# Kernel optimization log

Hardware: AMD Instinct MI355X
Metric: run time of the kernel (lower is better)

Reference implementation:

```python
import jax, jax.numpy as jnp
import numpy as np

C = 256
H_HEADS = 8
HEAD_DIM = C // H_HEADS
B, H, W = 2, 64, 64


def conv1x1(x, w, b):
    # x: [B,C,H,W], w: [O,C], b: [O]
    return jnp.einsum('oc,bchw->bohw', w, x) + b[None, :, None, None]


def setup_inputs() -> dict:
    key = jax.random.key(0)
    ks = jax.random.split(key, 12)
    s = 1.0 / np.sqrt(C)
    inp = {
        'query': jax.random.normal(ks[0], (B, C, H, W), jnp.float32),
        'key': jax.random.normal(ks[1], (B, C, H, W), jnp.float32),
        'value': jax.random.normal(ks[2], (B, C, H, W), jnp.float32),
        'wq': jax.random.uniform(ks[3], (C, C), jnp.float32, -s, s),
        'bq': jax.random.uniform(ks[4], (C,), jnp.float32, -s, s),
        'wk': jax.random.uniform(ks[5], (C, C), jnp.float32, -s, s),
        'bk': jax.random.uniform(ks[6], (C,), jnp.float32, -s, s),
        'wv': jax.random.uniform(ks[7], (C, C), jnp.float32, -s, s),
        'bv': jax.random.uniform(ks[8], (C,), jnp.float32, -s, s),
        'wo': jax.random.uniform(ks[9], (C, C), jnp.float32, -s, s),
        'bo': jax.random.uniform(ks[10], (C,), jnp.float32, -s, s),
    }
    return inp


def reference(query, key, value, wq, bq, wk, bk, wv, bv, wo, bo):
    b, c, h, w = query.shape
    hw = h * w
    q = conv1x1(query, wq, bq).reshape(b, H_HEADS, HEAD_DIM, hw)  # [B,nh,hd,HW]
    k = conv1x1(key, wk, bk).reshape(b, H_HEADS, HEAD_DIM, hw)
    v = conv1x1(value, wv, bv).reshape(b, H_HEADS, HEAD_DIM, hw)
    # scores: [B,nh,HW,HW]
    scores = jnp.einsum('bhdq,bhdk->bqhk'.replace('q', 'i').replace('k', 'j'), q, k)  # placeholder avoided
    scores = jnp.einsum('bhdi,bhdj->bhij', q, k) / np.sqrt(HEAD_DIM).astype(np.float32)
    attn = jax.nn.softmax(scores, axis=-1)
    out = jnp.einsum('bhij,bhdj->bhdi', attn, v)  # [B,nh,hd,HW]
    out = out.reshape(b, c, h, w)
    return conv1x1(out, wo, bo)
```

## Files before the change

### kernel.cpp

```cpp
#include <hip/hip_runtime.h>
#include <hip/hip_bf16.h>

#define C_DIM 256
#define HW    4096
#define NH    8
#define HD    32

typedef unsigned short u16;
typedef __attribute__((ext_vector_type(8)))  short bf16x8;
typedef __attribute__((ext_vector_type(4)))  float f32x4;
typedef __attribute__((ext_vector_type(16))) float f32x16;

#define QSCALE 0.25503486f

#if __has_builtin(__builtin_amdgcn_exp2f)
#define EXP2(x) __builtin_amdgcn_exp2f(x)
#else
#define EXP2(x) exp2f(x)
#endif

__device__ __forceinline__ u16 f2bf(float x) {
  __hip_bfloat16 h = __float2bfloat16(x);
  return __builtin_bit_cast(u16, h);
}
__device__ __forceinline__ bf16x8 ld8(const u16* p) {
  return *(const bf16x8*)p;
}
__device__ __forceinline__ f32x16 zero16() {
  f32x16 z;
#pragma unroll
  for (int i = 0; i < 16; ++i) z[i] = 0.0f;
  return z;
}

__device__ __forceinline__ unsigned cvtpk(float lo, float hi) {
  unsigned r;
  asm("v_cvt_pk_bf16_f32 %0, %1, %2" : "=v"(r) : "v"(lo), "v"(hi));
  return r;
}

__device__ __forceinline__ void permswap(unsigned& a, unsigned& b) {
#if __has_builtin(__builtin_amdgcn_permlane32_swap)
  auto r = __builtin_amdgcn_permlane32_swap(a, b, false, false);
  a = r[0];
  b = r[1];
#else
  asm volatile("s_nop 1\n\tv_permlane32_swap_b32 %0, %1" : "+v"(a), "+v"(b));
#endif
}

__global__ __launch_bounds__(256) void cast_kernel(
    const float* __restrict__ xq, const float* __restrict__ xk, const float* __restrict__ xv,
    const float* __restrict__ wq, const float* __restrict__ wk,
    const float* __restrict__ wv, const float* __restrict__ wo,
    u16* __restrict__ xT, u16* __restrict__ Wbf) {
  const int z = blockIdx.z;
  const int tx = threadIdx.x, ty = threadIdx.y;
  if (z == 6) {
    int gid = (blockIdx.y * 128 + blockIdx.x) * 256 + ty * 32 + tx;
    int wi = gid >> 16, e = gid & 65535;
    const float* s = (wi == 0) ? wq : (wi == 1) ? wk : (wi == 2) ? wv : wo;
    Wbf[gid] = f2bf(s[e]);
    return;
  }
  __shared__ float lds[32][33];
  const int t = z >> 1, b = z & 1;
  const float* src = (t == 0) ? xq : (t == 1) ? xk : xv;
  const int p0 = blockIdx.x * 32, c0 = blockIdx.y * 32;
#pragma unroll
  for (int j = 0; j < 4; ++j) {
    int c = c0 + ty + j * 8;
    lds[ty + j * 8][tx] = src[(b * C_DIM + c) * HW + p0 + tx];
  }
  __syncthreads();
  u16* dst = xT + (t * 2 + b) * (HW * C_DIM);
#pragma unroll
  for (int j = 0; j < 4; ++j) {
    int p = p0 + ty + j * 8;
    dst[p * C_DIM + c0 + tx] = f2bf(lds[tx][ty + j * 8]);
  }
}

__global__ __launch_bounds__(256) void gemm_qkv_kernel(
    const u16* __restrict__ xT, const u16* __restrict__ Wbf,
    const float* __restrict__ bq, const float* __restrict__ bk,
    const float* __restrict__ bvb,
    u16* __restrict__ qws, u16* __restrict__ kws, u16* __restrict__ vtws) {
  const int lane = threadIdx.x & 63;
  const int wave = threadIdx.x >> 6;
  const int l15 = lane & 15, l4 = lane >> 4;
  const int z = blockIdx.z;
  if (z < 4) {
    const int which = z >> 1, b = z & 1;
    const int m0 = blockIdx.x * 64 + (wave >> 1) * 32;
    const int n0 = blockIdx.y * 64 + (wave & 1) * 32;
    const u16* A  = xT + (which * 2 + b) * (HW * C_DIM);
    const u16* Bw = Wbf + which * (C_DIM * C_DIM);
    f32x4 acc[2][2] = {};
#pragma unroll
    for (int k0 = 0; k0 < 256; k0 += 32) {
      bf16x8 a0 = ld8(A + (m0 + l15) * 256 + k0 + l4 * 8);
      bf16x8 a1 = ld8(A + (m0 + 16 + l15) * 256 + k0 + l4 * 8);
      bf16x8 b0 = ld8(Bw + (n0 + l15) * 256 + k0 + l4 * 8);
      bf16x8 b1 = ld8(Bw + (n0 + 16 + l15) * 256 + k0 + l4 * 8);
      acc[0][0] = __builtin_amdgcn_mfma_f32_16x16x32_bf16(a0, b0, acc[0][0], 0, 0, 0);
      acc[0][1] = __builtin_amdgcn_mfma_f32_16x16x32_bf16(a0, b1, acc[0][1], 0, 0, 0);
      acc[1][0] = __builtin_amdgcn_mfma_f32_16x16x32_bf16(a1, b0, acc[1][0], 0, 0, 0);
      acc[1][1] = __builtin_amdgcn_mfma_f32_16x16x32_bf16(a1, b1, acc[1][1], 0, 0, 0);
    }
    const float scale = (which == 0) ? QSCALE : 1.0f;
    const float* bias = (which == 0) ? bq : bk;
    u16* out = (which == 0) ? qws : kws;
#pragma unroll
    for (int nt = 0; nt < 2; ++nt) {
      int o = n0 + nt * 16 + l15;
      int hh = o >> 5, d = o & 31;
      float bv = bias[o];
#pragma unroll
      for (int mt = 0; mt < 2; ++mt) {
#pragma unroll
        for (int r = 0; r < 4; ++r) {
          int p = m0 + mt * 16 + l4 * 4 + r;
          out[((b * NH + hh) * HW + p) * HD + d] = f2bf((acc[mt][nt][r] + bv) * scale);
        }
      }
    }
  } else {
    const int b = z - 4;
    const int m0 = blockIdx.y * 64 + (wave >> 1) * 32;
    const int n0 = blockIdx.x * 64 + (wave & 1) * 32;
    const u16* A  = Wbf + 2 * (C_DIM * C_DIM);
    const u16* Bx = xT + (2 * 2 + b) * (HW * C_DIM);
    f32x4 acc[2][2] = {};
#pragma unroll
    for (int k0 = 0; k0 < 256; k0 += 32) {
      bf16x8 a0 = ld8(A + (m0 + l15) * 256 + k0 + l4 * 8);
      bf16x8 a1 = ld8(A + (m0 + 16 + l15) * 256 + k0 + l4 * 8);
      bf16x8 b0 = ld8(Bx + (n0 + l15) * 256 + k0 + l4 * 8);
      bf16x8 b1 = ld8(Bx + (n0 + 16 + l15) * 256 + k0 + l4 * 8);
      acc[0][0] = __builtin_amdgcn_mfma_f32_16x16x32_bf16(a0, b0, acc[0][0], 0, 0, 0);
      acc[0][1] = __builtin_amdgcn_mfma_f32_16x16x32_bf16(a0, b1, acc[0][1], 0, 0, 0);
      acc[1][0] = __builtin_amdgcn_mfma_f32_16x16x32_bf16(a1, b0, acc[1][0], 0, 0, 0);
      acc[1][1] = __builtin_amdgcn_mfma_f32_16x16x32_bf16(a1, b1, acc[1][1], 0, 0, 0);
    }
#pragma unroll
    for (int mt = 0; mt < 2; ++mt) {
#pragma unroll
      for (int r = 0; r < 4; ++r) {
        int o = m0 + mt * 16 + l4 * 4 + r;
        float bvv = bvb[o];
#pragma unroll
        for (int nt = 0; nt < 2; ++nt) {
          int p = n0 + nt * 16 + l15;
          vtws[(b * C_DIM + o) * HW + p] = f2bf(acc[mt][nt][r] + bvv);
        }
      }
    }
  }
}

__device__ __forceinline__ void tile_step(const f32x16& st, bf16x8 va0, bf16x8 va1,
                                          f32x16& acc, float& lsum) {
  float p[16];
#pragma unroll
  for (int r = 0; r < 16; ++r) p[r] = EXP2(st[r]);
  float s0 = (p[0] + p[1]) + (p[2] + p[3]);
  float s1 = (p[4] + p[5]) + (p[6] + p[7]);
  float s2 = (p[8] + p[9]) + (p[10] + p[11]);
  float s3 = (p[12] + p[13]) + (p[14] + p[15]);
  lsum += (s0 + s1) + (s2 + s3);
  unsigned pk[8];
#pragma unroll
  for (int rr = 0; rr < 8; ++rr) pk[rr] = cvtpk(p[2 * rr], p[2 * rr + 1]);
  permswap(pk[0], pk[2]);
  permswap(pk[1], pk[3]);
  permswap(pk[4], pk[6]);
  permswap(pk[5], pk[7]);
  union { unsigned u[4]; bf16x8 v; } pb0, pb1;
  pb0.u[0] = pk[0]; pb0.u[1] = pk[1]; pb0.u[2] = pk[2]; pb0.u[3] = pk[3];
  pb1.u[0] = pk[4]; pb1.u[1] = pk[5]; pb1.u[2] = pk[6]; pb1.u[3] = pk[7];
  __builtin_amdgcn_s_setprio(1);
  acc = __builtin_amdgcn_mfma_f32_32x32x16_bf16(va0, pb0.v, acc, 0, 0, 0);
  acc = __builtin_amdgcn_mfma_f32_32x32x16_bf16(va1, pb1.v, acc, 0, 0, 0);
  __builtin_amdgcn_s_setprio(0);
}

__global__ __launch_bounds__(256, 4) void attn_kernel(
    const u16* __restrict__ qws, const u16* __restrict__ kws,
    const u16* __restrict__ vtws, u16* __restrict__ attno) {
  const int lane = threadIdx.x & 63;
  const int sp = threadIdx.x >> 6;
  const int l5 = lane & 31, h5 = lane >> 5;
  const int bh = blockIdx.x;
  const int b = bh >> 3, h = bh & 7;
  const int q0 = blockIdx.y * 64;
  const u16* qb = qws + bh * (HW * HD);
  const u16* kb = kws + bh * (HW * HD);
  const u16* vb = vtws + (b * C_DIM + h * HD + l5) * HW;

  bf16x8 qA0 = ld8(qb + (q0 + l5) * HD + h5 * 8);
  bf16x8 qA1 = ld8(qb + (q0 + l5) * HD + 16 + h5 * 8);
  bf16x8 qB0 = ld8(qb + (q0 + 32 + l5) * HD + h5 * 8);
  bf16x8 qB1 = ld8(qb + (q0 + 32 + l5) * HD + 16 + h5 * 8);
  f32x16 accA = zero16(), accB = zero16();
  const f32x16 zv = zero16();
  float lsA = 0.0f, lsB = 0.0f;

  const int j_beg = sp * (HW / 4), j_end = j_beg + (HW / 4);
  bf16x8 kf0 = ld8(kb + (j_beg + l5) * HD + h5 * 8);
  bf16x8 kf1 = ld8(kb + (j_beg + l5) * HD + 16 + h5 * 8);
  for (int j0 = j_beg; j0 < j_end; j0 += 32) {
    bf16x8 va0 = ld8(vb + j0 + h5 * 8);
    bf16x8 va1 = ld8(vb + j0 + 16 + h5 * 8);
    f32x16 st = __builtin_amdgcn_mfma_f32_32x32x16_bf16(kf0, qA0, zv, 0, 0, 0);
    st = __builtin_amdgcn_mfma_f32_32x32x16_bf16(kf1, qA1, st, 0, 0, 0);
    const int jn = (j0 + 32 < j_end) ? j0 + 32 : j_beg;
    bf16x8 nk0 = ld8(kb + (jn + l5) * HD + h5 * 8);
    bf16x8 nk1 = ld8(kb + (jn + l5) * HD + 16 + h5 * 8);
    tile_step(st, va0, va1, accA, lsA);
    f32x16 st2 = __builtin_amdgcn_mfma_f32_32x32x16_bf16(kf0, qB0, zv, 0, 0, 0);
    st2 = __builtin_amdgcn_mfma_f32_32x32x16_bf16(kf1, qB1, st2, 0, 0, 0);
    kf0 = nk0; kf1 = nk1;
    tile_step(st2, va0, va1, accB, lsB);
  }

  __shared__ float redA[3][2][1024];
  __shared__ float redL[3][2][64];
  if (sp != 0) {
#pragma unroll
    for (int r = 0; r < 16; ++r) {
      int d = (r & 3) + 8 * (r >> 2) + 4 * h5;
      redA[sp - 1][0][d * 32 + l5] = accA[r];
      redA[sp - 1][1][d * 32 + l5] = accB[r];
    }
    redL[sp - 1][0][h5 * 32 + l5] = lsA;
    redL[sp - 1][1][h5 * 32 + l5] = lsB;
  }
  __syncthreads();
  if (sp == 0) {
#pragma unroll
    for (int r = 0; r < 16; ++r) {
      int d = (r & 3) + 8 * (r >> 2) + 4 * h5;
      accA[r] += (redA[0][0][d * 32 + l5] + redA[1][0][d * 32 + l5]) +
                 redA[2][0][d * 32 + l5];
      accB[r] += (redA[0][1][d * 32 + l5] + redA[1][1][d * 32 + l5]) +
                 redA[2][1][d * 32 + l5];
    }
    lsA += (redL[0][0][h5 * 32 + l5] + redL[1][0][h5 * 32 + l5]) +
           redL[2][0][h5 * 32 + l5];
    lsB += (redL[0][1][h5 * 32 + l5] + redL[1][1][h5 * 32 + l5]) +
           redL[2][1][h5 * 32 + l5];
    unsigned uaA = __builtin_bit_cast(unsigned, lsA), ubA = uaA;
    permswap(uaA, ubA);
    float totA = __builtin_bit_cast(float, uaA) + __builtin_bit_cast(float, ubA);
    unsigned uaB = __builtin_bit_cast(unsigned, lsB), ubB = uaB;
    permswap(uaB, ubB);
    float totB = __builtin_bit_cast(float, uaB) + __builtin_bit_cast(float, ubB);
    const float invA = 1.0f / totA, invB = 1.0f / totB;
    u16* obA = attno + (bh * HW + q0 + l5) * HD;
    u16* obB = attno + (bh * HW + q0 + 32 + l5) * HD;
#pragma unroll
    for (int r = 0; r < 16; ++r) {
      int d = (r & 3) + 8 * (r >> 2) + 4 * h5;
      obA[d] = f2bf(accA[r] * invA);
      obB[d] = f2bf(accB[r] * invB);
    }
  }
}

__global__ __launch_bounds__(256) void gemm_o_kernel(
    const u16* __restrict__ attno, const u16* __restrict__ Wbf,
    const float* __restrict__ bo, float* __restrict__ outp) {
  const int lane = threadIdx.x & 63;
  const int wave = threadIdx.x >> 6;
  const int l15 = lane & 15, l4 = lane >> 4;
  const int b = blockIdx.z;
  const int m0 = blockIdx.y * 64 + (wave >> 1) * 32;
  const int n0 = blockIdx.x * 64 + (wave & 1) * 32;
  const u16* A  = Wbf + 3 * (C_DIM * C_DIM);
  const u16* Bx = attno + b * (NH * HW * HD);
  f32x4 acc[2][2] = {};
#pragma unroll
  for (int k0 = 0; k0 < 256; k0 += 32) {
    int ks = k0 >> 5;
    bf16x8 a0 = ld8(A + (m0 + l15) * 256 + k0 + l4 * 8);
    bf16x8 a1 = ld8(A + (m0 + 16 + l15) * 256 + k0 + l4 * 8);
    bf16x8 b0 = ld8(Bx + (ks * HW + n0 + l15) * HD + l4 * 8);
    bf16x8 b1 = ld8(Bx + (ks * HW + n0 + 16 + l15) * HD + l4 * 8);
    acc[0][0] = __builtin_amdgcn_mfma_f32_16x16x32_bf16(a0, b0, acc[0][0], 0, 0, 0);
    acc[0][1] = __builtin_amdgcn_mfma_f32_16x16x32_bf16(a0, b1, acc[0][1], 0, 0, 0);
    acc[1][0] = __builtin_amdgcn_mfma_f32_16x16x32_bf16(a1, b0, acc[1][0], 0, 0, 0);
    acc[1][1] = __builtin_amdgcn_mfma_f32_16x16x32_bf16(a1, b1, acc[1][1], 0, 0, 0);
  }
#pragma unroll
  for (int mt = 0; mt < 2; ++mt) {
#pragma unroll
    for (int r = 0; r < 4; ++r) {
      int o = m0 + mt * 16 + l4 * 4 + r;
      float bvv = bo[o];
#pragma unroll
      for (int nt = 0; nt < 2; ++nt) {
        int p = n0 + nt * 16 + l15;
        outp[(b * C_DIM + o) * HW + p] = acc[mt][nt][r] + bvv;
      }
    }
  }
}

extern "C" void kernel_launch(void* const* d_in, const int* in_sizes, int n_in,
                              void* d_out, int out_size, void* d_ws, size_t ws_size,
                              hipStream_t stream) {
  const float* xq = (const float*)d_in[0];
  const float* xk = (const float*)d_in[1];
  const float* xv = (const float*)d_in[2];
  const float* wq = (const float*)d_in[3];
  const float* bq = (const float*)d_in[4];
  const float* wk = (const float*)d_in[5];
  const float* bk = (const float*)d_in[6];
  const float* wv = (const float*)d_in[7];
  const float* bv = (const float*)d_in[8];
  const float* wo = (const float*)d_in[9];
  const float* bo = (const float*)d_in[10];

  if (ws_size < 29884416u) return;
  char* ws = (char*)d_ws;
  u16* xT    = (u16*)(ws);
  u16* Wbf   = (u16*)(ws + 12582912);
  u16* qws   = (u16*)(ws + 13107200);
  u16* kws   = (u16*)(ws + 17301504);
  u16* vtws  = (u16*)(ws + 21495808);
  u16* attno = (u16*)(ws + 25690112);

  cast_kernel<<<dim3(128, 8, 7), dim3(32, 8), 0, stream>>>(xq, xk, xv, wq, wk, wv, wo, xT, Wbf);
  gemm_qkv_kernel<<<dim3(64, 4, 6), dim3(256), 0, stream>>>(xT, Wbf, bq, bk, bv, qws, kws, vtws);
  attn_kernel<<<dim3(16, 64), dim3(256), 0, stream>>>(qws, kws, vtws, attno);
  gemm_o_kernel<<<dim3(64, 4, 2), dim3(256), 0, stream>>>(attno, Wbf, bo, (float*)d_out);
}
```

Measured before the change: 110.1 us.

## Vectorize cast kernel, use dot2 row sums, halve attention query tile

The cast kernel now uses float4 loads and ushort4 stores over 128-pixel tiles, and the weight cast is vectorized. The softmax row sum is computed with bf16 dot2 instructions on the packed probabilities instead of scalar fp32 adds. The attention kernel processes 32 queries per block instead of 64, doubling the grid to 2048 blocks. This raises parallelism and cuts VALU work, but each block now reloads K/V for half as many queries, doubling K/V traffic, and row sums now come from bf16-rounded probabilities.

```diff
diff --git a/kernel.cpp b/kernel.cpp
--- a/kernel.cpp
+++ b/kernel.cpp
@@ -10,6 +10,7 @@
 typedef __attribute__((ext_vector_type(8)))  short bf16x8;
 typedef __attribute__((ext_vector_type(4)))  float f32x4;
 typedef __attribute__((ext_vector_type(16))) float f32x16;
+typedef __bf16 bf16x2_t __attribute__((ext_vector_type(2)));
 
 #define QSCALE 0.25503486f
 
@@ -19,6 +20,12 @@
 #define EXP2(x) exp2f(x)
 #endif
 
+#if __has_builtin(__builtin_amdgcn_fdot2_f32_bf16)
+#define HAVE_DOT2 1
+#else
+#define HAVE_DOT2 0
+#endif
+
 __device__ __forceinline__ u16 f2bf(float x) {
   __hip_bfloat16 h = __float2bfloat16(x);
   return __builtin_bit_cast(u16, h);
@@ -38,6 +45,14 @@
   asm("v_cvt_pk_bf16_f32 %0, %1, %2" : "=v"(r) : "v"(lo), "v"(hi));
   return r;
 }
+
+#if HAVE_DOT2
+__device__ __forceinline__ void dot2acc(unsigned pk2, float& l) {
+  l = __builtin_amdgcn_fdot2_f32_bf16(__builtin_bit_cast(bf16x2_t, pk2),
+                                      __builtin_bit_cast(bf16x2_t, 0x3F803F80u),
+                                      l, false);
+}
+#endif
 
 __device__ __forceinline__ void permswap(unsigned& a, unsigned& b) {
 #if __has_builtin(__builtin_amdgcn_permlane32_swap)
@@ -57,27 +72,40 @@
   const int z = blockIdx.z;
   const int tx = threadIdx.x, ty = threadIdx.y;
   if (z == 6) {
-    int gid = (blockIdx.y * 128 + blockIdx.x) * 256 + ty * 32 + tx;
+    int gid = ((blockIdx.y * 32 + blockIdx.x) * 256 + ty * 32 + tx) * 4;
     int wi = gid >> 16, e = gid & 65535;
     const float* s = (wi == 0) ? wq : (wi == 1) ? wk : (wi == 2) ? wv : wo;
-    Wbf[gid] = f2bf(s[e]);
+    float4 v = *(const float4*)&s[e];
+    ushort4 o;
+    o.x = f2bf(v.x); o.y = f2bf(v.y); o.z = f2bf(v.z); o.w = f2bf(v.w);
+    *(ushort4*)&Wbf[gid] = o;
     return;
   }
-  __shared__ float lds[32][33];
+  __shared__ float lds[128][33];
   const int t = z >> 1, b = z & 1;
   const float* src = (t == 0) ? xq : (t == 1) ? xk : xv;
-  const int p0 = blockIdx.x * 32, c0 = blockIdx.y * 32;
-#pragma unroll
-  for (int j = 0; j < 4; ++j) {
-    int c = c0 + ty + j * 8;
-    lds[ty + j * 8][tx] = src[(b * C_DIM + c) * HW + p0 + tx];
+  const int p0 = blockIdx.x * 128, c0 = blockIdx.y * 32;
+#pragma unroll
+  for (int jj = 0; jj < 4; ++jj) {
+    int c = ty + jj * 8;
+    float4 v = *(const float4*)&src[(b * C_DIM + c0 + c) * HW + p0 + tx * 4];
+    lds[tx * 4 + 0][c] = v.x;
+    lds[tx * 4 + 1][c] = v.y;
+    lds[tx * 4 + 2][c] = v.z;
+    lds[tx * 4 + 3][c] = v.w;
   }
   __syncthreads();
   u16* dst = xT + (t * 2 + b) * (HW * C_DIM);
 #pragma unroll
-  for (int j = 0; j < 4; ++j) {
-    int p = p0 + ty + j * 8;
-    dst[p * C_DIM + c0 + tx] = f2bf(lds[tx][ty + j * 8]);
+  for (int it = 0; it < 4; ++it) {
+    int idx = it * 256 + ty * 32 + tx;
+    int p = idx >> 3, cq = idx & 7;
+    ushort4 o;
+    o.x = f2bf(lds[p][cq * 4 + 0]);
+    o.y = f2bf(lds[p][cq * 4 + 1]);
+    o.z = f2bf(lds[p][cq * 4 + 2]);
+    o.w = f2bf(lds[p][cq * 4 + 3]);
+    *(ushort4*)&dst[(p0 + p) * C_DIM + c0 + cq * 4] = o;
   }
 }
 
@@ -164,14 +192,23 @@
   float p[16];
 #pragma unroll
   for (int r = 0; r < 16; ++r) p[r] = EXP2(st[r]);
+  unsigned pk[8];
+#pragma unroll
+  for (int rr = 0; rr < 8; ++rr) pk[rr] = cvtpk(p[2 * rr], p[2 * rr + 1]);
+#if HAVE_DOT2
+  float la = 0.0f, lb = 0.0f;
+#pragma unroll
+  for (int rr = 0; rr < 4; ++rr) dot2acc(pk[rr], la);
+#pragma unroll
+  for (int rr = 4; rr < 8; ++rr) dot2acc(pk[rr], lb);
+  lsum += la + lb;
+#else
   float s0 = (p[0] + p[1]) + (p[2] + p[3]);
   float s1 = (p[4] + p[5]) + (p[6] + p[7]);
   float s2 = (p[8] + p[9]) + (p[10] + p[11]);
   float s3 = (p[12] + p[13]) + (p[14] + p[15]);
   lsum += (s0 + s1) + (s2 + s3);
-  unsigned pk[8];
-#pragma unroll
-  for (int rr = 0; rr < 8; ++rr) pk[rr] = cvtpk(p[2 * rr], p[2 * rr + 1]);
+#endif
   permswap(pk[0], pk[2]);
   permswap(pk[1], pk[3]);
   permswap(pk[4], pk[6]);
@@ -193,18 +230,16 @@
   const int l5 = lane & 31, h5 = lane >> 5;
   const int bh = blockIdx.x;
   const int b = bh >> 3, h = bh & 7;
-  const int q0 = blockIdx.y * 64;
+  const int q0 = blockIdx.y * 32;
   const u16* qb = qws + bh * (HW * HD);
   const u16* kb = kws + bh * (HW * HD);
   const u16* vb = vtws + (b * C_DIM + h * HD + l5) * HW;
 
   bf16x8 qA0 = ld8(qb + (q0 + l5) * HD + h5 * 8);
   bf16x8 qA1 = ld8(qb + (q0 + l5) * HD + 16 + h5 * 8);
-  bf16x8 qB0 = ld8(qb + (q0 + 32 + l5) * HD + h5 * 8);
-  bf16x8 qB1 = ld8(qb + (q0 + 32 + l5) * HD + 16 + h5 * 8);
-  f32x16 accA = zero16(), accB = zero16();
+  f32x16 acc = zero16();
   const f32x16 zv = zero16();
-  float lsA = 0.0f, lsB = 0.0f;
+  float ls = 0.0f;
 
   const int j_beg = sp * (HW / 4), j_end = j_beg + (HW / 4);
   bf16x8 kf0 = ld8(kb + (j_beg + l5) * HD + h5 * 8);
@@ -217,53 +252,39 @@
     const int jn = (j0 + 32 < j_end) ? j0 + 32 : j_beg;
     bf16x8 nk0 = ld8(kb + (jn + l5) * HD + h5 * 8);
     bf16x8 nk1 = ld8(kb + (jn + l5) * HD + 16 + h5 * 8);
-    tile_step(st, va0, va1, accA, lsA);
-    f32x16 st2 = __builtin_amdgcn_mfma_f32_32x32x16_bf16(kf0, qB0, zv, 0, 0, 0);
-    st2 = __builtin_amdgcn_mfma_f32_32x32x16_bf16(kf1, qB1, st2, 0, 0, 0);
+    tile_step(st, va0, va1, acc, ls);
     kf0 = nk0; kf1 = nk1;
-    tile_step(st2, va0, va1, accB, lsB);
-  }
-
-  __shared__ float redA[3][2][1024];
-  __shared__ float redL[3][2][64];
+  }
+
+  __shared__ float redA[3][1024];
+  __shared__ float redL[3][64];
   if (sp != 0) {
 #pragma unroll
     for (int r = 0; r < 16; ++r) {
       int d = (r & 3) + 8 * (r >> 2) + 4 * h5;
-      redA[sp - 1][0][d * 32 + l5] = accA[r];
-      redA[sp - 1][1][d * 32 + l5] = accB[r];
-    }
-    redL[sp - 1][0][h5 * 32 + l5] = lsA;
-    redL[sp - 1][1][h5 * 32 + l5] = lsB;
+      redA[sp - 1][d * 32 + l5] = acc[r];
+    }
+    redL[sp - 1][h5 * 32 + l5] = ls;
   }
   __syncthreads();
   if (sp == 0) {
 #pragma unroll
     for (int r = 0; r < 16; ++r) {
       int d = (r & 3) + 8 * (r >> 2) + 4 * h5;
-      accA[r] += (redA[0][0][d * 32 + l5] + redA[1][0][d * 32 + l5]) +
-                 redA[2][0][d * 32 + l5];
-      accB[r] += (redA[0][1][d * 32 + l5] + redA[1][1][d * 32 + l5]) +
-                 redA[2][1][d * 32 + l5];
-    }
-    lsA += (redL[0][0][h5 * 32 + l5] + redL[1][0][h5 * 32 + l5]) +
-           redL[2][0][h5 * 32 + l5];
-    lsB += (redL[0][1][h5 * 32 + l5] + redL[1][1][h5 * 32 + l5]) +
-           redL[2][1][h5 * 32 + l5];
-    unsigned uaA = __builtin_bit_cast(unsigned, lsA), ubA = uaA;
-    permswap(uaA, ubA);
-    float totA = __builtin_bit_cast(float, uaA) + __builtin_bit_cast(float, ubA);
-    unsigned uaB = __builtin_bit_cast(unsigned, lsB), ubB = uaB;
-    permswap(uaB, ubB);
-    float totB = __builtin_bit_cast(float, uaB) + __builtin_bit_cast(float, ubB);
-    const float invA = 1.0f / totA, invB = 1.0f / totB;
-    u16* obA = attno + (bh * HW + q0 + l5) * HD;
-    u16* obB = attno + (bh * HW + q0 + 32 + l5) * HD;
+      acc[r] += (redA[0][d * 32 + l5] + redA[1][d * 32 + l5]) +
+                redA[2][d * 32 + l5];
+    }
+    ls += (redL[0][h5 * 32 + l5] + redL[1][h5 * 32 + l5]) +
+          redL[2][h5 * 32 + l5];
+    unsigned ua = __builtin_bit_cast(unsigned, ls), ub = ua;
+    permswap(ua, ub);
+    float tot = __builtin_bit_cast(float, ua) + __builtin_bit_cast(float, ub);
+    const float inv = 1.0f / tot;
+    u16* ob = attno + (bh * HW + q0 + l5) * HD;
 #pragma unroll
     for (int r = 0; r < 16; ++r) {
       int d = (r & 3) + 8 * (r >> 2) + 4 * h5;
-      obA[d] = f2bf(accA[r] * invA);
-      obB[d] = f2bf(accB[r] * invB);
+      ob[d] = f2bf(acc[r] * inv);
     }
   }
 }
@@ -331,8 +352,8 @@
   u16* vtws  = (u16*)(ws + 21495808);
   u16* attno = (u16*)(ws + 25690112);
 
-  cast_kernel<<<dim3(128, 8, 7), dim3(32, 8), 0, stream>>>(xq, xk, xv, wq, wk, wv, wo, xT, Wbf);
+  cast_kernel<<<dim3(32, 8, 7), dim3(32, 8), 0, stream>>>(xq, xk, xv, wq, wk, wv, wo, xT, Wbf);
   gemm_qkv_kernel<<<dim3(64, 4, 6), dim3(256), 0, stream>>>(xT, Wbf, bq, bk, bv, qws, kws, vtws);
-  attn_kernel<<<dim3(16, 64), dim3(256), 0, stream>>>(qws, kws, vtws, attno);
+  attn_kernel<<<dim3(16, 128), dim3(256), 0, stream>>>(qws, kws, vtws, attno);
   gemm_o_kernel<<<dim3(64, 4, 2), dim3(256), 0, stream>>>(attno, Wbf, bo, (float*)d_out);
 }
```

Result: slower. 144.6 us (+31.4%).
